# Kernel tuning notes

Hardware: AMD Instinct MI355X
Metric: run time of the kernel (lower is better)

The kernel has to match this reference:

```python
import jax, jax.numpy as jnp
import numpy as np
from jax import lax


def setup_inputs() -> dict:
    key = jax.random.key(0)
    k1, k2, k3, k4 = jax.random.split(key, 4)
    H = 2048
    L = 3
    hidden_states = jax.random.normal(k1, (2, 4096, H), dtype=jnp.float32)
    Win = jax.random.normal(k2, (3 * H, H), dtype=jnp.float32) * (H ** -0.5)
    conv_w = jax.random.normal(k3, (H, 1, L), dtype=jnp.float32) * (L ** -0.5)
    Wout = jax.random.normal(k4, (H, H), dtype=jnp.float32) * (H ** -0.5)
    return {"hidden_states": hidden_states, "Win": Win, "conv_w": conv_w, "Wout": Wout}


def reference(hidden_states, Win, conv_w, Wout):
    H = hidden_states.shape[-1]
    L = conv_w.shape[-1]
    BCx = jnp.einsum('bsh,oh->bso', hidden_states, Win)  # (b, s, 3H)
    B, C, x = jnp.split(BCx, 3, axis=-1)
    Bx = jnp.transpose(B * x, (0, 2, 1))  # (b, H, s)
    # depthwise causal conv: left-pad L-1 so output length == s (torch pads both
    # sides then slices [..., :seqlen]; left-only padding is equivalent)
    conv_out = lax.conv_general_dilated(
        Bx, conv_w, window_strides=(1,), padding=[(L - 1, 0)],
        feature_group_count=H, dimension_numbers=('NCH', 'OIH', 'NCH'))
    y = C * jnp.transpose(conv_out, (0, 2, 1))  # (b, s, H)
    return jnp.einsum('bsh,oh->bso', y, Wout)
```

## Files before the change

kernel.cpp:

```cpp
#include <hip/hip_runtime.h>
#include <hip/hip_bf16.h>

typedef unsigned short u16;
typedef __attribute__((ext_vector_type(8))) short bf16x8;
typedef __attribute__((ext_vector_type(4))) float f32x4;

static __device__ __forceinline__ u16 f2bf(float f) {
    unsigned u = __float_as_uint(f);
    unsigned r = (u + 0x7fffu + ((u >> 16) & 1u)) >> 16;
    return (u16)r;
}
static __device__ __forceinline__ float bf2f(u16 u) {
    return __uint_as_float(((unsigned)u) << 16);
}

static __device__ __forceinline__ void async_copy16(const void* gptr, void* lptr) {
    __builtin_amdgcn_global_load_lds(
        (const __attribute__((address_space(1))) void*)gptr,
        (__attribute__((address_space(3))) void*)lptr, 16, 0, 0);
}

__global__ __launch_bounds__(256)
void cvt_all(const float* __restrict__ a, const float* __restrict__ b,
             const float* __restrict__ c,
             u16* __restrict__ oa, u16* __restrict__ ob, u16* __restrict__ oc) {
    int blk = blockIdx.x;
    const float* src; u16* dst; long base;
    if (blk < 16384)      { src = a; dst = oa; base = blk; }
    else if (blk < 28672) { src = b; dst = ob; base = blk - 16384; }
    else                  { src = c; dst = oc; base = blk - 28672; }
    long i = (base * 256 + threadIdx.x) * 4;
    float4 f = *(const float4*)(src + i);
    u16 o[4] = { f2bf(f.x), f2bf(f.y), f2bf(f.z), f2bf(f.w) };
    *(uint2*)(dst + i) = *(const uint2*)o;
}

template<bool BF16_OUT>
__global__ __launch_bounds__(512, 2)
void gemm_bt8(const u16* __restrict__ A, const u16* __restrict__ B,
              void* __restrict__ Cout, int M, int N, int K) {
    __shared__ __align__(16) u16 lds[65536];

    const int t    = threadIdx.x;
    const int lane = t & 63;
    const int wm   = (t >> 6) >> 2;
    const int wn   = (t >> 6) & 3;
    const int l15  = lane & 15;
    const int hi   = lane >> 4;
    const int l7   = lane & 7;

    const int id   = blockIdx.y * gridDim.x + blockIdx.x;
    const int cpx  = gridDim.x >> 3;
    const int bx   = (id & 7) * cpx + ((id >> 3) % cpx);
    const int by   = (id >> 3) / cpx;
    const long rowA = (long)by * 256;
    const long rowB = (long)bx * 256;

    const int pl0 = t >> 3;
    const int slotcol = ((t & 7) ^ (pl0 & 7)) * 8;
    const u16* Asrc[2][2]; const u16* Bsrc[2][2];
#pragma unroll
    for (int h = 0; h < 2; h++) {
        int gA0 = h * 64 + pl0;
        int gA1 = 128 + h * 64 + pl0;
        Asrc[h][0] = A + (rowA + gA0) * (long)K + slotcol;
        Asrc[h][1] = A + (rowA + gA1) * (long)K + slotcol;
        int nB0 = (pl0 >> 5) * 64 + h * 32 + (pl0 & 31);
        Bsrc[h][0] = B + (rowB + nB0) * (long)K + slotcol;
        Bsrc[h][1] = B + (rowB + nB0 + 128) * (long)K + slotcol;
    }
    const int t8 = t * 8;

    auto STAGE_A = [&](int bufo, int h, int kk) {
        u16* d = lds + bufo + h * 8192 + t8;
        async_copy16(Asrc[h][0] + kk, d);
        async_copy16(Asrc[h][1] + kk, d + 4096);
    };
    auto STAGE_B = [&](int bufo, int h, int kk) {
        u16* d = lds + bufo + 16384 + h * 8192 + t8;
        async_copy16(Bsrc[h][0] + kk, d);
        async_copy16(Bsrc[h][1] + kk, d + 4096);
    };

    const int aBase = wm * 4096 + l15 * 64;
    const int bBase = 16384 + wn * 2048 + l15 * 64;
    const int sOff0 = (hi ^ l7) * 8;
    const int sOff1 = ((4 + hi) ^ l7) * 8;

    bf16x8 af[4][2], ba[2][2], bb[2][2];
    f32x4 acc[8][4] = {};

    auto LOAD_A2 = [&](int bufo, int Mq, int mb) {
        const u16* p = lds + bufo + Mq * 8192 + aBase + mb * 1024;
        af[mb][0]     = *(const bf16x8*)(p + sOff0);
        af[mb][1]     = *(const bf16x8*)(p + sOff1);
        af[mb + 1][0] = *(const bf16x8*)(p + 1024 + sOff0);
        af[mb + 1][1] = *(const bf16x8*)(p + 1024 + sOff1);
    };
    auto LOAD_B = [&](bf16x8 (&bg)[2][2], int bufo, int Nq) {
        const u16* p = lds + bufo + Nq * 8192 + bBase;
        bg[0][0] = *(const bf16x8*)(p + sOff0);
        bg[0][1] = *(const bf16x8*)(p + sOff1);
        bg[1][0] = *(const bf16x8*)(p + 1024 + sOff0);
        bg[1][1] = *(const bf16x8*)(p + 1024 + sOff1);
    };
    auto MFMA_H = [&](int Mq, int Nq, int mb, bf16x8 (&bg)[2][2]) {
        __builtin_amdgcn_s_setprio(1);
#pragma unroll
        for (int ks = 0; ks < 2; ks++)
#pragma unroll
            for (int m = mb; m < mb + 2; m++)
#pragma unroll
                for (int n = 0; n < 2; n++)
                    acc[Mq * 4 + m][Nq * 2 + n] =
                        __builtin_amdgcn_mfma_f32_16x16x32_bf16(
                            af[m][ks], bg[n][ks], acc[Mq * 4 + m][Nq * 2 + n],
                            0, 0, 0);
        __builtin_amdgcn_s_setprio(0);
    };

#define BAR()   __builtin_amdgcn_s_barrier()
#define SB()    __builtin_amdgcn_sched_barrier(0)
#define LGKM(n) do { asm volatile("s_waitcnt lgkmcnt(" #n ")" ::: "memory"); \
                     __builtin_amdgcn_sched_barrier(0); } while (0)
#define VM(n)   asm volatile("s_waitcnt vmcnt(" #n ")" ::: "memory")

#define TILE(BC, BN, KK)                                                     \
                                                              \
    LOAD_B(ba, BC, 0); LOAD_A2(BC, 0, 0); SB(); LOAD_A2(BC, 0, 2);           \
    STAGE_A(BN, 0, KK); VM(2);                                               \
    LGKM(4); MFMA_H(0, 0, 0, ba); LGKM(0); MFMA_H(0, 0, 2, ba); BAR();       \
                                                              \
    LOAD_B(bb, BC, 1);                                                       \
    STAGE_B(BN, 0, KK);                                                      \
    LGKM(0); MFMA_H(0, 1, 0, bb); MFMA_H(0, 1, 2, bb); BAR();                \
                                                              \
    LOAD_A2(BC, 1, 0); SB(); LOAD_A2(BC, 1, 2);                              \
    STAGE_A(BN, 1, KK);                                                      \
    LGKM(4); MFMA_H(1, 1, 0, bb); LGKM(0); MFMA_H(1, 1, 2, bb); BAR();       \
                                                              \
    STAGE_B(BN, 1, KK); VM(4);                                               \
    MFMA_H(1, 0, 0, ba); MFMA_H(1, 0, 2, ba); BAR();

    STAGE_A(0, 0, 0);  STAGE_B(0, 0, 0);
    STAGE_A(0, 1, 0);  STAGE_B(0, 1, 0);
    asm volatile("s_waitcnt vmcnt(0)" ::: "memory");
    BAR();

    const int NT = K >> 6;
#pragma unroll 1
    for (int i = 0; i < NT; i += 2) {
        int k1 = (i + 1) << 6;
        int k2 = (i + 2 < NT) ? (i + 2) << 6 : 0;
        TILE(0, 32768, k1);
        TILE(32768, 0, k2);
    }
    asm volatile("s_waitcnt vmcnt(0) lgkmcnt(0)" ::: "memory");

#undef TILE
#undef VM
#undef LGKM
#undef SB
#undef BAR

    const long crowBase = rowA + wm * 128 + hi * 4;
    const long ccolBase = rowB + wn * 64 + l15;
#pragma unroll
    for (int mi = 0; mi < 8; mi++) {
#pragma unroll
        for (int nj = 0; nj < 4; nj++) {
            long base = (crowBase + mi * 16) * N + ccolBase + nj * 16;
#pragma unroll
            for (int r = 0; r < 4; r++) {
                float v = acc[mi][nj][r];
                long idx = base + (long)r * N;
                if (BF16_OUT) ((u16*)Cout)[idx] = f2bf(v);
                else          ((float*)Cout)[idx] = v;
            }
        }
    }
}

union U16x8 { uint4 v; u16 u[8]; };

__global__ __launch_bounds__(256)
void conv_fuse(const u16* __restrict__ BCx, const float* __restrict__ cw,
               u16* __restrict__ y) {
    const int row = blockIdx.x;
    const int h0  = threadIdx.x * 8;
    const int sl  = row & 4095;
    const u16* r0 = BCx + (long)row * 6144;

    U16x8 B0, X0, C0, B1, X1, B2, X2;
    B0.v = *(const uint4*)(r0 + h0);
    C0.v = *(const uint4*)(r0 + 2048 + h0);
    X0.v = *(const uint4*)(r0 + 4096 + h0);
    if (sl >= 1) {
        B1.v = *(const uint4*)(r0 - 6144 + h0);
        X1.v = *(const uint4*)(r0 - 6144 + 4096 + h0);
    } else { B1.v = make_uint4(0,0,0,0); X1.v = make_uint4(0,0,0,0); }
    if (sl >= 2) {
        B2.v = *(const uint4*)(r0 - 12288 + h0);
        X2.v = *(const uint4*)(r0 - 12288 + 4096 + h0);
    } else { B2.v = make_uint4(0,0,0,0); X2.v = make_uint4(0,0,0,0); }

    U16x8 o;
#pragma unroll
    for (int i = 0; i < 8; i++) {
        int h = h0 + i;
        float bx0 = bf2f(B0.u[i]) * bf2f(X0.u[i]);
        float bx1 = bf2f(B1.u[i]) * bf2f(X1.u[i]);
        float bx2 = bf2f(B2.u[i]) * bf2f(X2.u[i]);
        float v = cw[h*3+2] * bx0 + cw[h*3+1] * bx1 + cw[h*3] * bx2;
        o.u[i] = f2bf(v * bf2f(C0.u[i]));
    }
    *(uint4*)(y + (long)row * 2048 + h0) = o.v;
}

extern "C" void kernel_launch(void* const* d_in, const int* in_sizes, int n_in,
                              void* d_out, int out_size, void* d_ws, size_t ws_size,
                              hipStream_t stream) {
    const float* hs   = (const float*)d_in[0];
    const float* Win  = (const float*)d_in[1];
    const float* cw   = (const float*)d_in[2];
    const float* Wout = (const float*)d_in[3];
    float* out = (float*)d_out;

    char* ws = (char*)d_ws;
    u16* hsb   = (u16*)(ws);
    u16* Winb  = (u16*)(ws +  33554432);
    u16* Woutb = (u16*)(ws +  58720256);
    u16* bcx   = (u16*)(ws +  67108864);
    u16* yb    = (u16*)(ws + 167772160);

    cvt_all<<<32768, 256, 0, stream>>>(hs, Win, Wout, hsb, Winb, Woutb);

    gemm_bt8<true ><<<dim3(24, 32), 512, 0, stream>>>(hsb, Winb, bcx, 8192, 6144, 2048);

    conv_fuse<<<8192, 256, 0, stream>>>(bcx, cw, yb);

    gemm_bt8<false><<<dim3(8, 32), 512, 0, stream>>>(yb, Woutb, out, 8192, 2048, 2048);
}
```

Measured before the change: 432.9 us.

## Make GEMM persistent over column tiles and batch conv and cast kernels

The GEMM becomes a 256-block persistent-style kernel. Each block owns one row tile and loops over a contiguous range of column tiles, with blocks grouped by blockIdx&7, presumably to map column ranges to XCDs. The B source pointers are retargeted before the last k-tile so prefetch continues across output tiles, and the epilogue runs inside the loop. The load schedule inside a tile is reordered: both A and B stage earlier, with a single vmcnt(0) wait. The conversion kernel processes 8 chunks per thread, and the conv kernel computes 4 rows per block, reusing the neighbouring B*x products. Together these aim to cut launch and tail overhead and improve L2 locality, at the cost of fewer blocks in flight and a stronger wait that may stall the pipeline.

Result: slower. 445.2 us (+2.8%).

```diff
diff --git a/kernel.cpp b/kernel.cpp
--- a/kernel.cpp
+++ b/kernel.cpp
@@ -24,15 +24,18 @@
 void cvt_all(const float* __restrict__ a, const float* __restrict__ b,
              const float* __restrict__ c,
              u16* __restrict__ oa, u16* __restrict__ ob, u16* __restrict__ oc) {
-    int blk = blockIdx.x;
-    const float* src; u16* dst; long base;
-    if (blk < 16384)      { src = a; dst = oa; base = blk; }
-    else if (blk < 28672) { src = b; dst = ob; base = blk - 16384; }
-    else                  { src = c; dst = oc; base = blk - 28672; }
-    long i = (base * 256 + threadIdx.x) * 4;
-    float4 f = *(const float4*)(src + i);
-    u16 o[4] = { f2bf(f.x), f2bf(f.y), f2bf(f.z), f2bf(f.w) };
-    *(uint2*)(dst + i) = *(const uint2*)o;
+#pragma unroll
+    for (int it = 0; it < 8; it++) {
+        long li = ((long)it << 20) + (long)blockIdx.x * 256 + threadIdx.x;
+        const float* src; u16* dst; long u;
+        if (li < 4194304)      { src = a; dst = oa; u = li; }
+        else if (li < 7340032) { src = b; dst = ob; u = li - 4194304; }
+        else                   { src = c; dst = oc; u = li - 7340032; }
+        long i = u * 4;
+        float4 f = *(const float4*)(src + i);
+        u16 o[4] = { f2bf(f.x), f2bf(f.y), f2bf(f.z), f2bf(f.w) };
+        *(uint2*)(dst + i) = *(const uint2*)o;
+    }
 }
 
 template<bool BF16_OUT>
@@ -49,26 +52,31 @@
     const int hi   = lane >> 4;
     const int l7   = lane & 7;
 
-    const int id   = blockIdx.y * gridDim.x + blockIdx.x;
-    const int cpx  = gridDim.x >> 3;
-    const int bx   = (id & 7) * cpx + ((id >> 3) % cpx);
-    const int by   = (id >> 3) / cpx;
-    const long rowA = (long)by * 256;
-    const long rowB = (long)bx * 256;
+    const int nCols = N >> 8;
+    const int TPB   = nCols >> 3;
+    const int xcd   = blockIdx.x & 7;
+    const int slot  = blockIdx.x >> 3;
+    const long rowA = (long)slot * 256;
+    long rowB = (long)xcd * TPB * 256;
 
     const int pl0 = t >> 3;
     const int slotcol = ((t & 7) ^ (pl0 & 7)) * 8;
-    const u16* Asrc[2][2]; const u16* Bsrc[2][2];
+    const u16* Asrc[2][2];
+    const u16* Bsrc[2][2];
 #pragma unroll
     for (int h = 0; h < 2; h++) {
-        int gA0 = h * 64 + pl0;
-        int gA1 = 128 + h * 64 + pl0;
-        Asrc[h][0] = A + (rowA + gA0) * (long)K + slotcol;
-        Asrc[h][1] = A + (rowA + gA1) * (long)K + slotcol;
-        int nB0 = (pl0 >> 5) * 64 + h * 32 + (pl0 & 31);
-        Bsrc[h][0] = B + (rowB + nB0) * (long)K + slotcol;
-        Bsrc[h][1] = B + (rowB + nB0 + 128) * (long)K + slotcol;
-    }
+        Asrc[h][0] = A + (rowA + h * 64 + pl0) * (long)K + slotcol;
+        Asrc[h][1] = A + (rowA + 128 + h * 64 + pl0) * (long)K + slotcol;
+    }
+    auto SET_B = [&](long rB) {
+#pragma unroll
+        for (int h = 0; h < 2; h++) {
+            int nb = (pl0 >> 5) * 64 + h * 32 + (pl0 & 31);
+            Bsrc[h][0] = B + (rB + nb) * (long)K + slotcol;
+            Bsrc[h][1] = Bsrc[h][0] + 128 * (long)K;
+        }
+    };
+    SET_B(rowB);
     const int t8 = t * 8;
 
     auto STAGE_A = [&](int bufo, int h, int kk) {
@@ -128,18 +136,17 @@
 #define TILE(BC, BN, KK)                                                     \
                                                               \
     LOAD_B(ba, BC, 0); LOAD_A2(BC, 0, 0); SB(); LOAD_A2(BC, 0, 2);           \
-    STAGE_A(BN, 0, KK); VM(2);                                               \
+    STAGE_A(BN, 0, KK); STAGE_B(BN, 0, KK);                                  \
     LGKM(4); MFMA_H(0, 0, 0, ba); LGKM(0); MFMA_H(0, 0, 2, ba); BAR();       \
                                                               \
     LOAD_B(bb, BC, 1);                                                       \
-    STAGE_B(BN, 0, KK);                                                      \
+    STAGE_B(BN, 1, KK); STAGE_A(BN, 1, KK);                                  \
     LGKM(0); MFMA_H(0, 1, 0, bb); MFMA_H(0, 1, 2, bb); BAR();                \
                                                               \
     LOAD_A2(BC, 1, 0); SB(); LOAD_A2(BC, 1, 2);                              \
-    STAGE_A(BN, 1, KK);                                                      \
     LGKM(4); MFMA_H(1, 1, 0, bb); LGKM(0); MFMA_H(1, 1, 2, bb); BAR();       \
                                                               \
-    STAGE_B(BN, 1, KK); VM(4);                                               \
+    VM(0);                                                                   \
     MFMA_H(1, 0, 0, ba); MFMA_H(1, 0, 2, ba); BAR();
 
     STAGE_A(0, 0, 0);  STAGE_B(0, 0, 0);
@@ -149,11 +156,42 @@
 
     const int NT = K >> 6;
 #pragma unroll 1
-    for (int i = 0; i < NT; i += 2) {
-        int k1 = (i + 1) << 6;
-        int k2 = (i + 2 < NT) ? (i + 2) << 6 : 0;
-        TILE(0, 32768, k1);
-        TILE(32768, 0, k2);
+    for (int j = 0; j < TPB; j++) {
+        const long rowBc = rowB;
+#pragma unroll 1
+        for (int i = 0; i < NT - 2; i += 2) {
+            TILE(0, 32768, (i + 1) << 6);
+            TILE(32768, 0, (i + 2) << 6);
+        }
+        TILE(0, 32768, (NT - 1) << 6);
+        if (j + 1 < TPB) { rowB += 256; SET_B(rowB); }
+        TILE(32768, 0, 0);
+
+        const long crowBase = rowA + wm * 128 + hi * 4;
+        const long ccolBase = rowBc + wn * 64 + l15;
+#pragma unroll
+        for (int mi = 0; mi < 8; mi++) {
+#pragma unroll
+            for (int nj = 0; nj < 4; nj++) {
+                long base = (crowBase + mi * 16) * N + ccolBase + nj * 16;
+#pragma unroll
+                for (int r = 0; r < 4; r++) {
+                    float v = acc[mi][nj][r];
+                    long idx = base + (long)r * N;
+                    if (BF16_OUT) ((u16*)Cout)[idx] = f2bf(v);
+                    else          ((float*)Cout)[idx] = v;
+                }
+            }
+        }
+        if (j + 1 < TPB) {
+#pragma unroll
+            for (int mi = 0; mi < 8; mi++)
+#pragma unroll
+                for (int nj = 0; nj < 4; nj++)
+#pragma unroll
+                    for (int r = 0; r < 4; r++)
+                        acc[mi][nj][r] = 0.0f;
+        }
     }
     asm volatile("s_waitcnt vmcnt(0) lgkmcnt(0)" ::: "memory");
 
@@ -162,23 +200,6 @@
 #undef LGKM
 #undef SB
 #undef BAR
-
-    const long crowBase = rowA + wm * 128 + hi * 4;
-    const long ccolBase = rowB + wn * 64 + l15;
-#pragma unroll
-    for (int mi = 0; mi < 8; mi++) {
-#pragma unroll
-        for (int nj = 0; nj < 4; nj++) {
-            long base = (crowBase + mi * 16) * N + ccolBase + nj * 16;
-#pragma unroll
-            for (int r = 0; r < 4; r++) {
-                float v = acc[mi][nj][r];
-                long idx = base + (long)r * N;
-                if (BF16_OUT) ((u16*)Cout)[idx] = f2bf(v);
-                else          ((float*)Cout)[idx] = v;
-            }
-        }
-    }
 }
 
 union U16x8 { uint4 v; u16 u[8]; };
@@ -186,35 +207,54 @@
 __global__ __launch_bounds__(256)
 void conv_fuse(const u16* __restrict__ BCx, const float* __restrict__ cw,
                u16* __restrict__ y) {
-    const int row = blockIdx.x;
-    const int h0  = threadIdx.x * 8;
-    const int sl  = row & 4095;
-    const u16* r0 = BCx + (long)row * 6144;
-
-    U16x8 B0, X0, C0, B1, X1, B2, X2;
-    B0.v = *(const uint4*)(r0 + h0);
-    C0.v = *(const uint4*)(r0 + 2048 + h0);
-    X0.v = *(const uint4*)(r0 + 4096 + h0);
-    if (sl >= 1) {
-        B1.v = *(const uint4*)(r0 - 6144 + h0);
-        X1.v = *(const uint4*)(r0 - 6144 + 4096 + h0);
-    } else { B1.v = make_uint4(0,0,0,0); X1.v = make_uint4(0,0,0,0); }
-    if (sl >= 2) {
-        B2.v = *(const uint4*)(r0 - 12288 + h0);
-        X2.v = *(const uint4*)(r0 - 12288 + 4096 + h0);
-    } else { B2.v = make_uint4(0,0,0,0); X2.v = make_uint4(0,0,0,0); }
-
-    U16x8 o;
+    const int r0 = blockIdx.x * 4;
+    const int h0 = threadIdx.x * 8;
+    const int batch = r0 >> 12;
+
+    U16x8 Bv[6], Xv[6], Cv[4];
+#pragma unroll
+    for (int ii = 0; ii < 6; ii++) {
+        int g = r0 - 2 + ii;
+        if (g >= 0 && (g >> 12) == batch) {
+            const u16* rp = BCx + (long)g * 6144;
+            Bv[ii].v = *(const uint4*)(rp + h0);
+            Xv[ii].v = *(const uint4*)(rp + 4096 + h0);
+        } else {
+            Bv[ii].v = make_uint4(0, 0, 0, 0);
+            Xv[ii].v = make_uint4(0, 0, 0, 0);
+        }
+    }
+#pragma unroll
+    for (int jj = 0; jj < 4; jj++)
+        Cv[jj].v = *(const uint4*)(BCx + (long)(r0 + jj) * 6144 + 2048 + h0);
+
+    float bx[6][8];
+#pragma unroll
+    for (int ii = 0; ii < 6; ii++)
+#pragma unroll
+        for (int i = 0; i < 8; i++)
+            bx[ii][i] = bf2f(Bv[ii].u[i]) * bf2f(Xv[ii].u[i]);
+
+    float w0[8], w1[8], w2[8];
 #pragma unroll
     for (int i = 0; i < 8; i++) {
         int h = h0 + i;
-        float bx0 = bf2f(B0.u[i]) * bf2f(X0.u[i]);
-        float bx1 = bf2f(B1.u[i]) * bf2f(X1.u[i]);
-        float bx2 = bf2f(B2.u[i]) * bf2f(X2.u[i]);
-        float v = cw[h*3+2] * bx0 + cw[h*3+1] * bx1 + cw[h*3] * bx2;
-        o.u[i] = f2bf(v * bf2f(C0.u[i]));
-    }
-    *(uint4*)(y + (long)row * 2048 + h0) = o.v;
+        w0[i] = cw[h * 3];
+        w1[i] = cw[h * 3 + 1];
+        w2[i] = cw[h * 3 + 2];
+    }
+
+#pragma unroll
+    for (int jj = 0; jj < 4; jj++) {
+        U16x8 o;
+#pragma unroll
+        for (int i = 0; i < 8; i++) {
+            float v = w2[i] * bx[jj + 2][i] + w1[i] * bx[jj + 1][i]
+                    + w0[i] * bx[jj][i];
+            o.u[i] = f2bf(v * bf2f(Cv[jj].u[i]));
+        }
+        *(uint4*)(y + (long)(r0 + jj) * 2048 + h0) = o.v;
+    }
 }
 
 extern "C" void kernel_launch(void* const* d_in, const int* in_sizes, int n_in,
@@ -233,11 +273,11 @@
     u16* bcx   = (u16*)(ws +  67108864);
     u16* yb    = (u16*)(ws + 167772160);
 
-    cvt_all<<<32768, 256, 0, stream>>>(hs, Win, Wout, hsb, Winb, Woutb);
-
-    gemm_bt8<true ><<<dim3(24, 32), 512, 0, stream>>>(hsb, Winb, bcx, 8192, 6144, 2048);
-
-    conv_fuse<<<8192, 256, 0, stream>>>(bcx, cw, yb);
-
-    gemm_bt8<false><<<dim3(8, 32), 512, 0, stream>>>(yb, Woutb, out, 8192, 2048, 2048);
-}
+    cvt_all<<<4096, 256, 0, stream>>>(hs, Win, Wout, hsb, Winb, Woutb);
+
+    gemm_bt8<true ><<<256, 512, 0, stream>>>(hsb, Winb, bcx, 8192, 6144, 2048);
+
+    conv_fuse<<<2048, 256, 0, stream>>>(bcx, cw, yb);
+
+    gemm_bt8<false><<<256, 512, 0, stream>>>(yb, Woutb, out, 8192, 2048, 2048);
+}
```
